# Kernel tuning notes

Hardware: AMD Instinct MI355X
Metric: run time of the kernel (lower is better)

Reference implementation:

```python
import jax, jax.numpy as jnp
import numpy as np


def setup_inputs() -> dict:
    key = jax.random.key(0)
    ks = jax.random.split(key, 12)
    B, Nq, Ns, NODES = 128, 16, 256, 3
    V, E, C, H, OUT, NA = 50000, 300, 1024, 8, 300, 5000
    s = 0.05
    return {
        "he_ques": jax.random.randint(ks[0], (B, Nq, NODES), 0, V),
        "he_kg": jax.random.randint(ks[1], (B, Ns, NODES), 0, V),
        "emb": jax.random.normal(ks[2], (V, E), jnp.float32) * s,
        "q2h_w": jax.random.normal(ks[3], (C, E * NODES), jnp.float32) * s,
        "q2h_b": jax.random.normal(ks[4], (C,), jnp.float32) * s,
        "k2h_w": jax.random.normal(ks[5], (C, E * NODES), jnp.float32) * s,
        "k2h_b": jax.random.normal(ks[6], (C,), jnp.float32) * s,
        "h2att_w": jax.random.normal(ks[7], (H, C), jnp.float32) * s,
        "h2att_b": jax.random.normal(ks[8], (H,), jnp.float32) * s,
        "fc_w": jax.random.normal(ks[9], (OUT, C * H), jnp.float32) * s,
        "fc_b": jax.random.normal(ks[10], (OUT,), jnp.float32) * s,
        "glove_cands": jax.random.normal(ks[11], (NA, OUT), jnp.float32) * s,
    }


def reference(he_ques, he_kg, emb, q2h_w, q2h_b, k2h_w, k2h_b,
              h2att_w, h2att_b, fc_w, fc_b, glove_cands):
    B, Nq, _ = he_ques.shape
    Ns = he_kg.shape[1]
    H, C = h2att_w.shape
    # embed node indices and flatten per-hyperedge: [B, N, nodes*E]
    hq = emb[he_ques].reshape(B, Nq, -1)
    hs = emb[he_kg].reshape(B, Ns, -1)
    # linear projections (dropout p=0 in eval)
    hq = hq @ q2h_w.T + q2h_b  # [B, Nq, C]
    hs = hs @ k2h_w.T + k2h_b  # [B, Ns, C]
    # bilinear attention logits: h2att(outer(hq, hs)) fused into one einsum
    # logits[b,h,q,s] = sum_c hq[b,q,c] * hs[b,s,c] * W[h,c] + b[h]
    logits = jnp.einsum('bqc,bsc,hc->bhqs', hq, hs, h2att_w) + h2att_b[None, :, None, None]
    att = jax.nn.softmax(logits.reshape(B, H, Nq * Ns), axis=2).reshape(B, H, Nq, Ns)
    # per-head bilinear readout (replaces the per-head repeat+matmul loop):
    # out[b,h,c] = sum_{q,s} hq[b,q,c] * att[b,h,q,s] * hs[b,s,c]
    pooled = jnp.einsum('bqc,bhqs,bsc->bhc', hq, att, hs).reshape(B, H * C)
    out = pooled @ fc_w.T + fc_b  # [B, n_out]
    sim = out @ glove_cands.T  # [B, n_ans]
    return jax.nn.log_softmax(sim, axis=1)
```

## Files before the change

### kernel.cpp

```cpp
#include <hip/hip_runtime.h>
#include <stdint.h>


typedef short s16x8 __attribute__((ext_vector_type(8)));
typedef float f32x4 __attribute__((ext_vector_type(4)));

#define ASYNC_CP16(gsrc, ldst)                                                  \
  __builtin_amdgcn_global_load_lds(                                             \
      (const __attribute__((address_space(1))) void*)(gsrc),                    \
      (__attribute__((address_space(3))) void*)(ldst), 16, 0, 0)

__device__ __forceinline__ float bfr2f(uint16_t u) {
  return __builtin_bit_cast(float, (uint32_t)u << 16);
}
__device__ __forceinline__ uint16_t f2bfr(float f) {
  uint32_t u = __builtin_bit_cast(uint32_t, f);
  u += 0x7fffu + ((u >> 16) & 1u);
  return (uint16_t)(u >> 16);
}

__global__ __launch_bounds__(256) void cvt_all(
    const float* __restrict__ emb_f, const float* __restrict__ wk_f,
    const float* __restrict__ wq_f, const float* __restrict__ glove_f,
    const float* __restrict__ watt_f,
    uint16_t* __restrict__ EMB, uint16_t* __restrict__ WK,
    uint16_t* __restrict__ WQ, uint16_t* __restrict__ GLV,
    uint16_t* __restrict__ WATT) {
  const int idx = blockIdx.x * 256 + threadIdx.x;
  const int TOT = 61264 * 80;
  if (idx < TOT) {
    const int row = idx / 80, j = idx % 80;
    const float* src;
    uint16_t* dst;
    int srow, svalid;
    if (row < 50000) {
      src = emb_f; dst = EMB; srow = row; svalid = 1;
    } else if (row < 53072) {
      src = wk_f; dst = WK + (size_t)(row - 50000) * 0; srow = row - 50000;
      dst = WK; svalid = 1;
    } else if (row < 56144) {
      src = wq_f; dst = WQ; srow = row - 53072; svalid = 1;
    } else {
      src = glove_f; dst = GLV; srow = row - 56144; svalid = (srow < 5000);
    }
    float4 v = make_float4(0.f, 0.f, 0.f, 0.f);
    if (svalid && j < 75) v = *(const float4*)(src + (size_t)srow * 300 + j * 4);
    ushort4 o;
    o.x = f2bfr(v.x); o.y = f2bfr(v.y); o.z = f2bfr(v.z); o.w = f2bfr(v.w);
    const int drow = (row < 50000) ? row : srow;
    *(ushort4*)(dst + (size_t)drow * 320 + j * 4) = o;
  } else {
    const int i = idx - TOT;
    if (i < 1024) {
      float4 a = *(const float4*)(watt_f + i * 8);
      float4 b = *(const float4*)(watt_f + i * 8 + 4);
      ushort4 o0, o1;
      o0.x = f2bfr(a.x); o0.y = f2bfr(a.y); o0.z = f2bfr(a.z); o0.w = f2bfr(a.w);
      o1.x = f2bfr(b.x); o1.y = f2bfr(b.y); o1.z = f2bfr(b.z); o1.w = f2bfr(b.w);
      *(ushort4*)(WATT + i * 8) = o0;
      *(ushort4*)(WATT + i * 8 + 4) = o1;
    }
  }
}

__global__ __launch_bounds__(256) void cvt_fc(const float* __restrict__ src,
                                              uint16_t* __restrict__ dst) {
  int i4 = blockIdx.x * 256 + threadIdx.x;
  int pos = i4 * 4;
  int r = pos >> 13, c = pos & 8191;
  float4 v = make_float4(0.f, 0.f, 0.f, 0.f);
  if (r < 300) v = *(const float4*)(src + (size_t)r * 8192 + c);
  ushort4 o;
  o.x = f2bfr(v.x); o.y = f2bfr(v.y); o.z = f2bfr(v.z); o.w = f2bfr(v.w);
  *(ushort4*)(dst + (size_t)r * 8192 + c) = o;
}

__global__ __launch_bounds__(256) void gemm_gather2(
    const int* __restrict__ heK, const int* __restrict__ heQ,
    const uint16_t* __restrict__ emb,
    const uint16_t* __restrict__ WKp, const uint16_t* __restrict__ WQp,
    const float* __restrict__ bK, const float* __restrict__ bQ,
    uint16_t* __restrict__ HS, uint16_t* __restrict__ HQ) {
  __shared__ uint16_t ring[3 * 8192];
  __shared__ int sIdx[384];
  char* ringB = (char*)ring;

  const int t = threadIdx.x;
  const int lane = t & 63, wave = t >> 6;
  const int wr = wave >> 1, wc = wave & 1;
  const int fr = lane & 15, fq = lane >> 4;
  const int srow = t >> 2, skg = t & 3;
  const int skg2 = skg ^ ((srow >> 1) & 3);

  const int v = blockIdx.x + 8 * blockIdx.y;
  const int w = (v & 7) * 272 + (v >> 3);
  const int bx = w & 7, by = w >> 3;
  const int n0 = bx * 128;
  const bool isK = by < 256;
  const int m0 = (isK ? by : by - 256) * 128;
  const int* he = isK ? heK : heQ;
  const uint16_t* W = isK ? WKp : WQp;
  const float* bias = isK ? bK : bQ;
  uint16_t* C = isK ? HS : HQ;

  for (int i = t; i < 384; i += 256) sIdx[i] = he[(long)m0 * 3 + i];
  __syncthreads();

  uint32_t ea[2][3];
#pragma unroll
  for (int h = 0; h < 2; h++)
#pragma unroll
    for (int nd = 0; nd < 3; nd++)
      ea[h][nd] =
          (uint32_t)sIdx[(h * 64 + srow) * 3 + nd] * 640u + (uint32_t)(skg2 * 16);
  const uint16_t* Wr0 = W + (long)(n0 + srow) * 960 + skg2 * 8;
  const uint16_t* Wr1 = W + (long)(n0 + 64 + srow) * 960 + skg2 * 8;

  f32x4 zv = {0.f, 0.f, 0.f, 0.f};
  f32x4 acc[4][4];
#pragma unroll
  for (int i = 0; i < 4; i++)
#pragma unroll
    for (int j = 0; j < 4; j++) acc[i][j] = zv;

  int snd = 0, skk = 0, sk = 0, sbuf = 0;
  auto STAGE = [&]() {
    const int bb = sbuf * 16384;
    const uint32_t e0 = snd == 0 ? ea[0][0] : (snd == 1 ? ea[0][1] : ea[0][2]);
    const uint32_t e1 = snd == 0 ? ea[1][0] : (snd == 1 ? ea[1][1] : ea[1][2]);
    ASYNC_CP16((const char*)emb + e0 + skk * 64, ringB + bb + t * 16);
    ASYNC_CP16((const char*)emb + e1 + skk * 64, ringB + bb + 4096 + t * 16);
    ASYNC_CP16(Wr0 + sk, ringB + bb + 8192 + t * 16);
    ASYNC_CP16(Wr1 + sk, ringB + bb + 12288 + t * 16);
    sk += 32;
    if (++skk == 10) { skk = 0; ++snd; }
    if (++sbuf == 3) sbuf = 0;
  };

  STAGE();
  STAGE();

  const int fsw = (fq ^ ((fr >> 1) & 3)) * 8;
  int aof[4], bof[4];
#pragma unroll
  for (int mi = 0; mi < 4; mi++) aof[mi] = (wr * 64 + mi * 16 + fr) * 32 + fsw;
#pragma unroll
  for (int ni = 0; ni < 4; ni++)
    bof[ni] = 4096 + (wc * 64 + ni * 16 + fr) * 32 + fsw;

  int cbuf = 0;
  for (int kt = 0; kt < 30; ++kt) {
    if (kt < 28) STAGE();
    if (kt < 28)      asm volatile("s_waitcnt vmcnt(8)" ::: "memory");
    else if (kt < 29) asm volatile("s_waitcnt vmcnt(4)" ::: "memory");
    else              asm volatile("s_waitcnt vmcnt(0)" ::: "memory");
    __builtin_amdgcn_s_barrier();
    asm volatile("" ::: "memory");
    const uint16_t* base = ring + cbuf * 8192;
    s16x8 af[4], bv[4];
#pragma unroll
    for (int mi = 0; mi < 4; mi++) af[mi] = *(const s16x8*)(base + aof[mi]);
#pragma unroll
    for (int ni = 0; ni < 4; ni++) bv[ni] = *(const s16x8*)(base + bof[ni]);
    __builtin_amdgcn_s_setprio(1);
#pragma unroll
    for (int mi = 0; mi < 4; mi++)
#pragma unroll
      for (int ni = 0; ni < 4; ni++)
        acc[mi][ni] = __builtin_amdgcn_mfma_f32_16x16x32_bf16(
            af[mi], bv[ni], acc[mi][ni], 0, 0, 0);
    __builtin_amdgcn_s_setprio(0);
    asm volatile("s_waitcnt lgkmcnt(0)" ::: "memory");
    __builtin_amdgcn_s_barrier();
    if (++cbuf == 3) cbuf = 0;
  }

#pragma unroll
  for (int ni = 0; ni < 4; ni++) {
    const int gn = n0 + wc * 64 + ni * 16 + fr;
    const float bval = bias[gn];
#pragma unroll
    for (int mi = 0; mi < 4; mi++) {
      const int gmb = m0 + wr * 64 + mi * 16 + fq * 4;
      uint16_t* cp = C + (long)gmb * 1024 + gn;
      cp[0]    = f2bfr(acc[mi][ni][0] + bval);
      cp[1024] = f2bfr(acc[mi][ni][1] + bval);
      cp[2048] = f2bfr(acc[mi][ni][2] + bval);
      cp[3072] = f2bfr(acc[mi][ni][3] + bval);
    }
  }
}

__global__ __launch_bounds__(256) void gemm_logits(
    const uint16_t* __restrict__ hq, const uint16_t* __restrict__ watt,
    const uint16_t* __restrict__ hs, uint16_t* __restrict__ att) {
  __shared__ uint16_t ring[3 * 4096];
  char* ringB = (char*)ring;

  const int t = threadIdx.x;
  const int lane = t & 63, wave = t >> 6;
  const int wr = wave >> 1, wc = wave & 1;
  const int fr = lane & 15, fq = lane >> 4;
  const int srow = t >> 2, skg = t & 3;
  const int skg2 = skg ^ ((srow >> 1) & 3);

  int bx = blockIdx.x, bz = blockIdx.z;
  {
    const int v = bx + 2 * bz;
    const int w = (v & 7) * 32 + (v >> 3);
    bx = w & 1;
    bz = w >> 1;
  }
  const int n0 = bx * 128;

  const uint16_t* Bs0 = hs + (long)bz * 262144 + (long)(n0 + srow) * 1024 + skg2 * 8;
  const uint16_t* Bs1 = hs + (long)bz * 262144 + (long)(n0 + 64 + srow) * 1024 + skg2 * 8;
  const uint16_t* hqp = hq + (long)(bz * 16 + fr) * 1024 + fq * 8;
  const uint16_t* wp0 = watt + (long)(wr * 4 + 0) * 1024 + fq * 8;
  const uint16_t* wp1 = watt + (long)(wr * 4 + 1) * 1024 + fq * 8;
  const uint16_t* wp2 = watt + (long)(wr * 4 + 2) * 1024 + fq * 8;
  const uint16_t* wp3 = watt + (long)(wr * 4 + 3) * 1024 + fq * 8;

  f32x4 zv = {0.f, 0.f, 0.f, 0.f};
  f32x4 acc[4][4];
#pragma unroll
  for (int i = 0; i < 4; i++)
#pragma unroll
    for (int j = 0; j < 4; j++) acc[i][j] = zv;

  int sbuf = 0, cbuf = 0;
  ASYNC_CP16(Bs0, ringB + t * 16);
  ASYNC_CP16(Bs1, ringB + 2048 + t * 16);
  ASYNC_CP16(Bs0 + 32, ringB + 4096 + t * 16);
  ASYNC_CP16(Bs1 + 32, ringB + 4096 + 2048 + t * 16);
  sbuf = 2;
  s16x8 hqA = *(const s16x8*)(hqp);
  s16x8 wA0 = *(const s16x8*)(wp0), wA1 = *(const s16x8*)(wp1);
  s16x8 wA2 = *(const s16x8*)(wp2), wA3 = *(const s16x8*)(wp3);
  s16x8 hqB, wB0, wB1, wB2, wB3;

  const int fsw = (fq ^ ((fr >> 1) & 3)) * 8;
  int bof[4];
#pragma unroll
  for (int ni = 0; ni < 4; ni++)
    bof[ni] = (wc * 64 + ni * 16 + fr) * 32 + fsw;

#define LOG_BODY(KT, HQS, W0S, W1S, W2S, W3S, HQD, W0D, W1D, W2D, W3D)          \
  {                                                                             \
    const int kt = (KT);                                                        \
    if (kt + 2 < 32) {                                                          \
      ASYNC_CP16(Bs0 + (kt + 2) * 32, ringB + sbuf * 4096 + t * 16);            \
      ASYNC_CP16(Bs1 + (kt + 2) * 32, ringB + sbuf * 4096 + 2048 + t * 16);     \
      if (++sbuf == 3) sbuf = 0;                                                \
    }                                                                           \
    if (kt + 1 < 32) {                                                          \
      const int ko = (kt + 1) * 32;                                             \
      HQD = *(const s16x8*)(hqp + ko);                                          \
      W0D = *(const s16x8*)(wp0 + ko); W1D = *(const s16x8*)(wp1 + ko);         \
      W2D = *(const s16x8*)(wp2 + ko); W3D = *(const s16x8*)(wp3 + ko);         \
    }                                                                           \
    asm volatile("s_waitcnt vmcnt(7)" ::: "memory");                            \
    __builtin_amdgcn_s_barrier();                                               \
    asm volatile("" ::: "memory");                                              \
    s16x8 af0, af1, af2, af3, bv[4];                                            \
    _Pragma("unroll") for (int j = 0; j < 8; j++) {                             \
      const float hv = bfr2f((uint16_t)HQS[j]);                                 \
      af0[j] = (short)f2bfr(hv * bfr2f((uint16_t)W0S[j]));                      \
      af1[j] = (short)f2bfr(hv * bfr2f((uint16_t)W1S[j]));                      \
      af2[j] = (short)f2bfr(hv * bfr2f((uint16_t)W2S[j]));                      \
      af3[j] = (short)f2bfr(hv * bfr2f((uint16_t)W3S[j]));                      \
    }                                                                           \
    const uint16_t* base = ring + cbuf * 4096;                                  \
    _Pragma("unroll") for (int ni = 0; ni < 4; ni++)                            \
        bv[ni] = *(const s16x8*)(base + bof[ni]);                               \
    __builtin_amdgcn_s_setprio(1);                                              \
    _Pragma("unroll") for (int ni = 0; ni < 4; ni++) {                          \
      acc[0][ni] = __builtin_amdgcn_mfma_f32_16x16x32_bf16(af0, bv[ni],         \
                                                           acc[0][ni], 0, 0, 0);\
      acc[1][ni] = __builtin_amdgcn_mfma_f32_16x16x32_bf16(af1, bv[ni],         \
                                                           acc[1][ni], 0, 0, 0);\
      acc[2][ni] = __builtin_amdgcn_mfma_f32_16x16x32_bf16(af2, bv[ni],         \
                                                           acc[2][ni], 0, 0, 0);\
      acc[3][ni] = __builtin_amdgcn_mfma_f32_16x16x32_bf16(af3, bv[ni],         \
                                                           acc[3][ni], 0, 0, 0);\
    }                                                                           \
    __builtin_amdgcn_s_setprio(0);                                              \
    asm volatile("s_waitcnt lgkmcnt(0)" ::: "memory");                          \
    __builtin_amdgcn_s_barrier();                                               \
    if (++cbuf == 3) cbuf = 0;                                                  \
  }

  for (int kt2 = 0; kt2 < 32; kt2 += 2) {
    LOG_BODY(kt2, hqA, wA0, wA1, wA2, wA3, hqB, wB0, wB1, wB2, wB3);
    LOG_BODY(kt2 + 1, hqB, wB0, wB1, wB2, wB3, hqA, wA0, wA1, wA2, wA3);
  }
#undef LOG_BODY

#pragma unroll
  for (int ni = 0; ni < 4; ni++) {
    const int gn = n0 + wc * 64 + ni * 16 + fr;
#pragma unroll
    for (int mi = 0; mi < 4; mi++)
#pragma unroll
      for (int j = 0; j < 4; j++) {
        const int gm = wr * 64 + mi * 16 + fq * 4 + j;
        att[(long)bz * 32768 + gm * 256 + gn] = f2bfr(acc[mi][ni][j]);
      }
  }
}

template <int SWZ>
__global__ __launch_bounds__(256) void gemm_pipe(
    const uint16_t* __restrict__ A, int lda, long sAb,
    const uint16_t* __restrict__ Bt, int ldb, long sBb,
    int ksteps, int kchunk,
    float* __restrict__ Cf, int ldcf, int nmax, long sCf) {
  __shared__ uint16_t ring[3 * 8192];
  char* ringB = (char*)ring;

  const int t = threadIdx.x;
  const int lane = t & 63, wave = t >> 6;
  const int wr = wave >> 1, wc = wave & 1;
  const int fr = lane & 15, fq = lane >> 4;
  const int srow = t >> 2, skg = t & 3;
  const int skg2 = skg ^ ((srow >> 1) & 3);

  int bx = blockIdx.x, bz = blockIdx.z;
  if (SWZ) {
    const int nwg = gridDim.x * gridDim.z;
    const int v = bx + gridDim.x * bz;
    const int w = (v & 7) * (nwg >> 3) + (v >> 3);
    bx = w % gridDim.x;
    bz = w / gridDim.x;
  }
  const int m0 = blockIdx.y * 128, n0 = bx * 128;
  const uint16_t* Ab = A + (long)bz * sAb;
  const uint16_t* Bb = Bt;

  f32x4 zv = {0.f, 0.f, 0.f, 0.f};
  f32x4 acc[4][4];
#pragma unroll
  for (int i = 0; i < 4; i++)
#pragma unroll
    for (int j = 0; j < 4; j++) acc[i][j] = zv;

  const long kbase = (long)bz * kchunk;
  const uint16_t* As0 = Ab + (long)(m0 + srow) * lda + kbase + skg2 * 8;
  const uint16_t* As1 = Ab + (long)(m0 + 64 + srow) * lda + kbase + skg2 * 8;
  const uint16_t* Bs0 = Bb + (long)(n0 + srow) * ldb + kbase + skg2 * 8;
  const uint16_t* Bs1 = Bb + (long)(n0 + 64 + srow) * ldb + kbase + skg2 * 8;

  int sk = 0, sbuf = 0;
  auto STAGE = [&]() {
    const int bb = sbuf * 16384;
    ASYNC_CP16(As0 + sk, ringB + bb + t * 16);
    ASYNC_CP16(As1 + sk, ringB + bb + 4096 + t * 16);
    ASYNC_CP16(Bs0 + sk, ringB + bb + 8192 + t * 16);
    ASYNC_CP16(Bs1 + sk, ringB + bb + 12288 + t * 16);
    sk += 32;
    if (++sbuf == 3) sbuf = 0;
  };

  STAGE();
  STAGE();

  const int fsw = (fq ^ ((fr >> 1) & 3)) * 8;
  int aof[4], bof[4];
#pragma unroll
  for (int mi = 0; mi < 4; mi++) aof[mi] = (wr * 64 + mi * 16 + fr) * 32 + fsw;
#pragma unroll
  for (int ni = 0; ni < 4; ni++)
    bof[ni] = 4096 + (wc * 64 + ni * 16 + fr) * 32 + fsw;

  int cbuf = 0;
  for (int kt = 0; kt < ksteps; ++kt) {
    if (kt + 2 < ksteps) STAGE();
    if (kt + 2 < ksteps)      asm volatile("s_waitcnt vmcnt(8)" ::: "memory");
    else if (kt + 1 < ksteps) asm volatile("s_waitcnt vmcnt(4)" ::: "memory");
    else                      asm volatile("s_waitcnt vmcnt(0)" ::: "memory");
    __builtin_amdgcn_s_barrier();
    asm volatile("" ::: "memory");
    const uint16_t* base = ring + cbuf * 8192;
    s16x8 af[4], bv[4];
#pragma unroll
    for (int mi = 0; mi < 4; mi++) af[mi] = *(const s16x8*)(base + aof[mi]);
#pragma unroll
    for (int ni = 0; ni < 4; ni++) bv[ni] = *(const s16x8*)(base + bof[ni]);
#pragma unroll
    for (int mi = 0; mi < 4; mi++)
#pragma unroll
      for (int ni = 0; ni < 4; ni++)
        acc[mi][ni] = __builtin_amdgcn_mfma_f32_16x16x32_bf16(
            af[mi], bv[ni], acc[mi][ni], 0, 0, 0);
    asm volatile("s_waitcnt lgkmcnt(0)" ::: "memory");
    __builtin_amdgcn_s_barrier();
    if (++cbuf == 3) cbuf = 0;
  }

#pragma unroll
  for (int ni = 0; ni < 4; ni++) {
    const int gn = n0 + wc * 64 + ni * 16 + fr;
    if (gn < nmax) {
#pragma unroll
      for (int mi = 0; mi < 4; mi++)
#pragma unroll
        for (int j = 0; j < 4; j++) {
          const int gm = m0 + wr * 64 + mi * 16 + fq * 4 + j;
          Cf[(long)bz * sCf + (long)gm * ldcf + gn] = acc[mi][ni][j];
        }
    }
  }
}

__global__ __launch_bounds__(256) void gemm_pv(
    const uint16_t* __restrict__ att, const uint16_t* __restrict__ hs,
    const uint16_t* __restrict__ hqp, uint16_t* __restrict__ pooled) {
  __shared__ uint16_t sT[128 * 264];
  __shared__ uint16_t sA[4096];
  __shared__ uint16_t sHq[2048];

  const int t = threadIdx.x;
  const int lane = t & 63, wave = t >> 6;
  const int wr = wave >> 1, wc = wave & 1;
  const int fr = lane & 15, fq = lane >> 4;
  const int srow = t >> 2, skg = t & 3;
  const int skg2 = skg ^ ((srow >> 1) & 3);

  int bx = blockIdx.x, bz = blockIdx.z;
  {
    const int v = bx + 8 * bz;
    const int w = (v & 7) * 128 + (v >> 3);
    bx = w & 7;
    bz = w >> 3;
  }
  const int n0 = bx * 128;

  const uint16_t* hsb = hs + (long)bz * 262144;
  const int sloc = t & 15, c8 = t >> 4;
  s16x8 vv[16];
#pragma unroll
  for (int p = 0; p < 16; p++)
    vv[p] = *(const s16x8*)(hsb + (long)(p * 16 + sloc) * 1024 + n0 + c8 * 8);
  *(s16x8*)(sHq + (t >> 4) * 128 + (t & 15) * 8) =
      *(const s16x8*)(hqp + (long)bz * 16384 + (long)(t >> 4) * 1024 + n0 +
                      (t & 15) * 8);
#pragma unroll
  for (int p = 0; p < 16; p++) {
    const int s = p * 16 + sloc;
#pragma unroll
    for (int j = 0; j < 8; j++)
      sT[(c8 * 8 + j) * 264 + s] = (uint16_t)vv[p][j];
  }
  __syncthreads();

  f32x4 zv = {0.f, 0.f, 0.f, 0.f};
  f32x4 acc[4][4];
#pragma unroll
  for (int i = 0; i < 4; i++)
#pragma unroll
    for (int j = 0; j < 4; j++) acc[i][j] = zv;

  const uint16_t* As0 = att + (long)bz * 32768 + (long)srow * 256 + skg2 * 8;
  const uint16_t* As1 = att + (long)bz * 32768 + (long)(64 + srow) * 256 + skg2 * 8;

  const int fsw = (fq ^ ((fr >> 1) & 3)) * 8;
  int aof[4];
#pragma unroll
  for (int mi = 0; mi < 4; mi++) aof[mi] = (wr * 64 + mi * 16 + fr) * 32 + fsw;

  for (int kt = 0; kt < 8; ++kt) {
    ASYNC_CP16(As0 + kt * 32, (char*)sA + t * 16);
    ASYNC_CP16(As1 + kt * 32, (char*)sA + 4096 + t * 16);
    __syncthreads();
    s16x8 af[4], bv[4];
#pragma unroll
    for (int mi = 0; mi < 4; mi++) af[mi] = *(const s16x8*)(sA + aof[mi]);
#pragma unroll
    for (int ni = 0; ni < 4; ni++)
      bv[ni] = *(const s16x8*)(sT + (wc * 64 + ni * 16 + fr) * 264 + kt * 32 +
                               fq * 8);
    __builtin_amdgcn_s_setprio(1);
#pragma unroll
    for (int mi = 0; mi < 4; mi++)
#pragma unroll
      for (int ni = 0; ni < 4; ni++)
        acc[mi][ni] = __builtin_amdgcn_mfma_f32_16x16x32_bf16(
            af[mi], bv[ni], acc[mi][ni], 0, 0, 0);
    __builtin_amdgcn_s_setprio(0);
    __syncthreads();
  }

#pragma unroll
  for (int mi = 0; mi < 4; mi++) {
    const int hh = wr * 4 + mi;
#pragma unroll
    for (int ni = 0; ni < 4; ni++) {
      const int col = wc * 64 + ni * 16 + fr;
      float p = 0.f;
#pragma unroll
      for (int j = 0; j < 4; j++)
        p += acc[mi][ni][j] * bfr2f(sHq[(fq * 4 + j) * 128 + col]);
      p += __shfl_xor(p, 16);
      p += __shfl_xor(p, 32);
      if (fq == 0)
        pooled[(long)bz * 8192 + hh * 1024 + n0 + col] = f2bfr(p);
    }
  }
}

__global__ __launch_bounds__(256) void softmax_att(uint16_t* __restrict__ att) {
  const int b = blockIdx.x >> 3, h = blockIdx.x & 7;
  uint16_t* base = att + (long)b * 32768 + h * 4096;
  const int t = threadIdx.x;
  __shared__ float red[8];
  s16x8 v0 = *(const s16x8*)(base + t * 16);
  s16x8 v1 = *(const s16x8*)(base + t * 16 + 8);
  float f[16];
#pragma unroll
  for (int j = 0; j < 8; j++) {
    f[j] = bfr2f((uint16_t)v0[j]);
    f[8 + j] = bfr2f((uint16_t)v1[j]);
  }
  float mx = f[0];
#pragma unroll
  for (int j = 1; j < 16; j++) mx = fmaxf(mx, f[j]);
#pragma unroll
  for (int d = 1; d < 64; d <<= 1) mx = fmaxf(mx, __shfl_xor(mx, d));
  if ((t & 63) == 0) red[t >> 6] = mx;
  __syncthreads();
  mx = fmaxf(fmaxf(red[0], red[1]), fmaxf(red[2], red[3]));
  float s = 0.f;
#pragma unroll
  for (int j = 0; j < 16; j++) {
    f[j] = __expf(f[j] - mx);
    s += f[j];
  }
#pragma unroll
  for (int d = 1; d < 64; d <<= 1) s += __shfl_xor(s, d);
  if ((t & 63) == 0) red[4 + (t >> 6)] = s;
  __syncthreads();
  const float ri = 1.f / (red[4] + red[5] + red[6] + red[7]);
  s16x8 o0, o1;
#pragma unroll
  for (int j = 0; j < 8; j++) {
    o0[j] = (short)f2bfr(f[j] * ri);
    o1[j] = (short)f2bfr(f[8 + j] * ri);
  }
  *(s16x8*)(base + t * 16) = o0;
  *(s16x8*)(base + t * 16 + 8) = o1;
}

__global__ __launch_bounds__(256) void cvt_out_k(const float* __restrict__ parts,
                                                 const float* __restrict__ fc_b,
                                                 uint16_t* __restrict__ outb) {
  int idx = blockIdx.x * 256 + threadIdx.x;
  if (idx >= 128 * 320) return;
  int m = idx / 320, n = idx % 320;
  float v = 0.f;
  if (n < 300) {
    v = fc_b[n];
#pragma unroll
    for (int ch = 0; ch < 32; ch++) v += parts[ch * 38400 + m * 300 + n];
  }
  outb[idx] = f2bfr(v);
}

__global__ __launch_bounds__(256) void logsoftmax_k(const float* __restrict__ sim,
                                                    float* __restrict__ out) {
  const int r = blockIdx.x, t = threadIdx.x;
  __shared__ float red[4];
  __shared__ float red2[4];
  const float* x = sim + (long)r * 5000;
  float mx = -1e30f;
  for (int i = t; i < 5000; i += 256) mx = fmaxf(mx, x[i]);
#pragma unroll
  for (int d = 1; d < 64; d <<= 1) mx = fmaxf(mx, __shfl_xor(mx, d));
  if ((t & 63) == 0) red[t >> 6] = mx;
  __syncthreads();
  mx = fmaxf(fmaxf(red[0], red[1]), fmaxf(red[2], red[3]));
  float s = 0.f;
  for (int i = t; i < 5000; i += 256) s += __expf(x[i] - mx);
#pragma unroll
  for (int d = 1; d < 64; d <<= 1) s += __shfl_xor(s, d);
  if ((t & 63) == 0) red2[t >> 6] = s;
  __syncthreads();
  s = red2[0] + red2[1] + red2[2] + red2[3];
  const float lse = mx + logf(s);
  float* o = out + (long)r * 5000;
  for (int i = t; i < 5000; i += 256) o[i] = x[i] - lse;
}

extern "C" void kernel_launch(void* const* d_in, const int* in_sizes, int n_in,
                              void* d_out, int out_size, void* d_ws, size_t ws_size,
                              hipStream_t stream) {
  (void)in_sizes; (void)n_in; (void)out_size; (void)ws_size;
  const int* he_q = (const int*)d_in[0];
  const int* he_k = (const int*)d_in[1];
  const float* emb_f = (const float*)d_in[2];
  const float* q2h_w = (const float*)d_in[3];
  const float* q2h_b = (const float*)d_in[4];
  const float* k2h_w = (const float*)d_in[5];
  const float* k2h_b = (const float*)d_in[6];
  const float* h2att_w = (const float*)d_in[7];
  const float* fc_w = (const float*)d_in[9];
  const float* fc_b = (const float*)d_in[10];
  const float* glove = (const float*)d_in[11];
  float* out = (float*)d_out;

  char* ws = (char*)d_ws;
  uint16_t* EMB   = (uint16_t*)(ws);
  uint16_t* WK    = (uint16_t*)(ws + 32000000);
  uint16_t* WQ    = (uint16_t*)(ws + 33966080);
  uint16_t* WATT  = (uint16_t*)(ws + 35932160);
  uint16_t* WFC   = (uint16_t*)(ws + 35948544);
  uint16_t* GLV   = (uint16_t*)(ws + 42240000);
  uint16_t* HQ    = (uint16_t*)(ws + 45516800);
  uint16_t* HS    = (uint16_t*)(ws + 49711104);
  uint16_t* ATT   = (uint16_t*)(ws + 183928832);
  uint16_t* POOL  = (uint16_t*)(ws + 192317440);
  uint16_t* OUTB  = (uint16_t*)(ws + 195643392);
  float*    SIM   = (float*)(ws + 195725312);
  float*    PARTS = (float*)(ws + 49711104);

  cvt_all<<<19149, 256, 0, stream>>>(emb_f, k2h_w, q2h_w, glove, h2att_w,
                                     EMB, WK, WQ, GLV, WATT);
  cvt_fc<<<3072, 256, 0, stream>>>(fc_w, WFC);

  gemm_gather2<<<dim3(8, 272), 256, 0, stream>>>(
      he_k, he_q, EMB, WK, WQ, k2h_b, q2h_b, HS, HQ);

  gemm_logits<<<dim3(2, 1, 128), 256, 0, stream>>>(HQ, WATT, HS, ATT);
  softmax_att<<<1024, 256, 0, stream>>>(ATT);

  gemm_pv<<<dim3(8, 1, 128), 256, 0, stream>>>(ATT, HS, HQ, POOL);

  gemm_pipe<0><<<dim3(3, 1, 32), 256, 0, stream>>>(
      POOL, 8192, 0, WFC, 8192, 0, 8, 256, PARTS, 300, 300, 38400);

  cvt_out_k<<<160, 256, 0, stream>>>(PARTS, fc_b, OUTB);

  gemm_pipe<0><<<dim3(40, 1, 1), 256, 0, stream>>>(
      OUTB, 320, 0, GLV, 320, 0, 10, 0, SIM, 5000, 5000, 0);

  logsoftmax_k<<<128, 256, 0, stream>>>(SIM, out);
}
```

Before: 209.0 us.

## Load gather GEMM operands directly from global into registers, dropping LDS ring

The gathered-embedding projection GEMM no longer stages A and B tiles through a triple-buffered LDS ring filled by async global-to-LDS copies. Each wave now loads its MFMA fragments straight from global memory, using per-lane row offsets computed from the gathered indices, and the 30 k-steps are fully unrolled. This removes the LDS traffic, barriers and waitcnt bookkeeping. In exchange, operand reuse across waves is lost, so each fragment is fetched from global/L2 by two waves, and the compiler must hide load latency without an explicit pipeline. A small cleanup in the conversion kernel simplifies the destination-row logic.

```diff
diff --git a/kernel.cpp b/kernel.cpp
--- a/kernel.cpp
+++ b/kernel.cpp
@@ -36,8 +36,7 @@
     if (row < 50000) {
       src = emb_f; dst = EMB; srow = row; svalid = 1;
     } else if (row < 53072) {
-      src = wk_f; dst = WK + (size_t)(row - 50000) * 0; srow = row - 50000;
-      dst = WK; svalid = 1;
+      src = wk_f; dst = WK; srow = row - 50000; svalid = 1;
     } else if (row < 56144) {
       src = wq_f; dst = WQ; srow = row - 53072; svalid = 1;
     } else {
@@ -47,8 +46,7 @@
     if (svalid && j < 75) v = *(const float4*)(src + (size_t)srow * 300 + j * 4);
     ushort4 o;
     o.x = f2bfr(v.x); o.y = f2bfr(v.y); o.z = f2bfr(v.z); o.w = f2bfr(v.w);
-    const int drow = (row < 50000) ? row : srow;
-    *(ushort4*)(dst + (size_t)drow * 320 + j * 4) = o;
+    *(ushort4*)(dst + (size_t)srow * 320 + j * 4) = o;
   } else {
     const int i = idx - TOT;
     if (i < 1024) {
@@ -75,22 +73,18 @@
   *(ushort4*)(dst + (size_t)r * 8192 + c) = o;
 }
 
-__global__ __launch_bounds__(256) void gemm_gather2(
+__global__ __launch_bounds__(256) void gemm_gather3(
     const int* __restrict__ heK, const int* __restrict__ heQ,
     const uint16_t* __restrict__ emb,
     const uint16_t* __restrict__ WKp, const uint16_t* __restrict__ WQp,
     const float* __restrict__ bK, const float* __restrict__ bQ,
     uint16_t* __restrict__ HS, uint16_t* __restrict__ HQ) {
-  __shared__ uint16_t ring[3 * 8192];
   __shared__ int sIdx[384];
-  char* ringB = (char*)ring;
 
   const int t = threadIdx.x;
   const int lane = t & 63, wave = t >> 6;
   const int wr = wave >> 1, wc = wave & 1;
   const int fr = lane & 15, fq = lane >> 4;
-  const int srow = t >> 2, skg = t & 3;
-  const int skg2 = skg ^ ((srow >> 1) & 3);
 
   const int v = blockIdx.x + 8 * blockIdx.y;
   const int w = (v & 7) * 272 + (v >> 3);
@@ -106,15 +100,22 @@
   for (int i = t; i < 384; i += 256) sIdx[i] = he[(long)m0 * 3 + i];
   __syncthreads();
 
-  uint32_t ea[2][3];
-#pragma unroll
-  for (int h = 0; h < 2; h++)
-#pragma unroll
-    for (int nd = 0; nd < 3; nd++)
-      ea[h][nd] =
-          (uint32_t)sIdx[(h * 64 + srow) * 3 + nd] * 640u + (uint32_t)(skg2 * 16);
-  const uint16_t* Wr0 = W + (long)(n0 + srow) * 960 + skg2 * 8;
-  const uint16_t* Wr1 = W + (long)(n0 + 64 + srow) * 960 + skg2 * 8;
+  uint32_t aoff[3][4];
+#pragma unroll
+  for (int nd = 0; nd < 3; nd++)
+#pragma unroll
+    for (int mi = 0; mi < 4; mi++)
+      aoff[nd][mi] =
+          (uint32_t)sIdx[(wr * 64 + mi * 16 + fr) * 3 + nd] * 640u +
+          (uint32_t)(fq * 16);
+  uint32_t boff[4];
+#pragma unroll
+  for (int ni = 0; ni < 4; ni++)
+    boff[ni] = (uint32_t)(n0 + wc * 64 + ni * 16 + fr) * 1920u +
+               (uint32_t)(fq * 16);
+
+  const char* embB = (const char*)emb;
+  const char* wB = (const char*)W;
 
   f32x4 zv = {0.f, 0.f, 0.f, 0.f};
   f32x4 acc[4][4];
@@ -123,56 +124,24 @@
 #pragma unroll
     for (int j = 0; j < 4; j++) acc[i][j] = zv;
 
-  int snd = 0, skk = 0, sk = 0, sbuf = 0;
-  auto STAGE = [&]() {
-    const int bb = sbuf * 16384;
-    const uint32_t e0 = snd == 0 ? ea[0][0] : (snd == 1 ? ea[0][1] : ea[0][2]);
-    const uint32_t e1 = snd == 0 ? ea[1][0] : (snd == 1 ? ea[1][1] : ea[1][2]);
-    ASYNC_CP16((const char*)emb + e0 + skk * 64, ringB + bb + t * 16);
-    ASYNC_CP16((const char*)emb + e1 + skk * 64, ringB + bb + 4096 + t * 16);
-    ASYNC_CP16(Wr0 + sk, ringB + bb + 8192 + t * 16);
-    ASYNC_CP16(Wr1 + sk, ringB + bb + 12288 + t * 16);
-    sk += 32;
-    if (++skk == 10) { skk = 0; ++snd; }
-    if (++sbuf == 3) sbuf = 0;
-  };
-
-  STAGE();
-  STAGE();
-
-  const int fsw = (fq ^ ((fr >> 1) & 3)) * 8;
-  int aof[4], bof[4];
-#pragma unroll
-  for (int mi = 0; mi < 4; mi++) aof[mi] = (wr * 64 + mi * 16 + fr) * 32 + fsw;
-#pragma unroll
-  for (int ni = 0; ni < 4; ni++)
-    bof[ni] = 4096 + (wc * 64 + ni * 16 + fr) * 32 + fsw;
-
-  int cbuf = 0;
-  for (int kt = 0; kt < 30; ++kt) {
-    if (kt < 28) STAGE();
-    if (kt < 28)      asm volatile("s_waitcnt vmcnt(8)" ::: "memory");
-    else if (kt < 29) asm volatile("s_waitcnt vmcnt(4)" ::: "memory");
-    else              asm volatile("s_waitcnt vmcnt(0)" ::: "memory");
-    __builtin_amdgcn_s_barrier();
-    asm volatile("" ::: "memory");
-    const uint16_t* base = ring + cbuf * 8192;
-    s16x8 af[4], bv[4];
-#pragma unroll
-    for (int mi = 0; mi < 4; mi++) af[mi] = *(const s16x8*)(base + aof[mi]);
-#pragma unroll
-    for (int ni = 0; ni < 4; ni++) bv[ni] = *(const s16x8*)(base + bof[ni]);
-    __builtin_amdgcn_s_setprio(1);
-#pragma unroll
-    for (int mi = 0; mi < 4; mi++)
+#pragma unroll
+  for (int nd = 0; nd < 3; nd++) {
+#pragma unroll
+    for (int kk = 0; kk < 10; kk++) {
+      s16x8 af[4], bv[4];
+#pragma unroll
+      for (int mi = 0; mi < 4; mi++)
+        af[mi] = *(const s16x8*)(embB + (size_t)aoff[nd][mi] + kk * 64);
 #pragma unroll
       for (int ni = 0; ni < 4; ni++)
-        acc[mi][ni] = __builtin_amdgcn_mfma_f32_16x16x32_bf16(
-            af[mi], bv[ni], acc[mi][ni], 0, 0, 0);
-    __builtin_amdgcn_s_setprio(0);
-    asm volatile("s_waitcnt lgkmcnt(0)" ::: "memory");
-    __builtin_amdgcn_s_barrier();
-    if (++cbuf == 3) cbuf = 0;
+        bv[ni] = *(const s16x8*)(wB + (size_t)boff[ni] + nd * 640 + kk * 64);
+#pragma unroll
+      for (int mi = 0; mi < 4; mi++)
+#pragma unroll
+        for (int ni = 0; ni < 4; ni++)
+          acc[mi][ni] = __builtin_amdgcn_mfma_f32_16x16x32_bf16(
+              af[mi], bv[ni], acc[mi][ni], 0, 0, 0);
+    }
   }
 
 #pragma unroll
@@ -626,7 +595,7 @@
                                      EMB, WK, WQ, GLV, WATT);
   cvt_fc<<<3072, 256, 0, stream>>>(fc_w, WFC);
 
-  gemm_gather2<<<dim3(8, 272), 256, 0, stream>>>(
+  gemm_gather3<<<dim3(8, 272), 256, 0, stream>>>(
       he_k, he_q, EMB, WK, WQ, k2h_b, q2h_b, HS, HQ);
 
   gemm_logits<<<dim3(2, 1, 128), 256, 0, stream>>>(HQ, WATT, HS, ATT);
```

Result: slower. 357.5 us (+71.1%).
